# Optimization experiments

Measured on AMD Instinct MI355X. Metric: run time of the kernel, lower is better.

The kernel has to match this reference:

```python
import jax, jax.numpy as jnp
import numpy as np

B, L, D, H = 4, 2048, 1024, 16
DK = D // H  # 64


def setup_inputs() -> dict:
    key = jax.random.key(0)
    ks = jax.random.split(key, 8)
    s = 0.05
    return {
        "query": jax.random.normal(ks[0], (B, L, D), jnp.float32),
        "key": jax.random.normal(ks[1], (B, L, D), jnp.float32),
        "value": jax.random.normal(ks[2], (B, L, D), jnp.float32),
        "mask": jnp.ones((B, L, L), jnp.int32),
        "Wq": jax.random.normal(ks[3], (D, DK), jnp.float32) * s,
        "Wk": jax.random.normal(ks[4], (D, DK), jnp.float32) * s,
        "Wv": jax.random.normal(ks[5], (D, DK), jnp.float32) * s,
        "Wo": jax.random.normal(ks[6], (H * DK, D), jnp.float32) * s,
    }


def reference(query, key, value, mask, Wq, Wk, Wv, Wo):
    # Single-head projections (the torch module projects once, then reuses
    # the SAME q/k/v for every head, producing num_heads identical outputs).
    q = jnp.einsum("bld,dk->blk", query, Wq)   # [B, L, DK]
    k = jnp.einsum("bld,dk->blk", key, Wk)
    v = jnp.einsum("bld,dk->blk", value, Wv)
    scale = 1.0 / jnp.sqrt(jnp.asarray(DK, q.dtype))
    scores = jnp.einsum("bqk,bsk->bqs", q, k) * scale  # [B, L, L]
    scores = jnp.where(mask == 0, -jnp.inf, scores)
    p = jax.nn.softmax(scores, axis=-1)
    head = jnp.einsum("bqs,bsk->bqk", p, v)    # [B, L, DK]
    # Concatenation of H identical heads == tile along last dim.
    out = jnp.tile(head, (1, 1, H))             # [B, L, H*DK]
    return jnp.einsum("blh,hd->bld", out, Wo)
```

## Files before the change

### kernel.cpp

```cpp
#include <hip/hip_runtime.h>
#include <hip/hip_bf16.h>

#define Bb 4
#define Ll 2048
#define Dd 1024
#define DKk 64
#define BL (Bb*Ll)
#define G_SPLIT 8
#define KSPLIT 4

typedef __attribute__((ext_vector_type(4))) float f32x4;
typedef __attribute__((ext_vector_type(8))) short bf16x8;

__device__ __forceinline__ unsigned short f2bf(float x) {
  unsigned int u = __builtin_bit_cast(unsigned int, x);
  u += 0x7fffu + ((u >> 16) & 1u);
  return (unsigned short)(u >> 16);
}
__device__ __forceinline__ unsigned int pack2bf(float a, float b) {
  return (unsigned int)f2bf(a) | ((unsigned int)f2bf(b) << 16);
}

__global__ __launch_bounds__(256)
void prep_kernel(const float* __restrict__ Wq, const float* __restrict__ Wk,
                 const float* __restrict__ Wv, const float* __restrict__ Wo,
                 unsigned short* __restrict__ Wfq, unsigned short* __restrict__ Wfk,
                 unsigned short* __restrict__ Wfv, unsigned short* __restrict__ WoSumT) {
  int idx = blockIdx.x * 256 + threadIdx.x;
  if (idx < 3 * 65536) {
    int which = idx >> 16;
    int r = idx & 65535;
    int n = r & 63, k = r >> 6;
    const float* W = which == 0 ? Wq : (which == 1 ? Wk : Wv);
    unsigned short* Wf = which == 0 ? Wfq : (which == 1 ? Wfk : Wfv);
    const int t = n >> 4, lr = n & 15;
    const int kidx = k >> 5, g = (k >> 3) & 3, e = k & 7;
    Wf[(size_t)(((kidx * 4 + t) * 4 + g) * 128) + lr * 8 + e] = f2bf(W[(size_t)k * 64 + n]);
  } else {
    int r = idx - 3 * 65536;
    int d = r & 1023, k = r >> 10;
    float s = 0.f;
#pragma unroll
    for (int h = 0; h < 16; ++h) s += Wo[(size_t)(h * 64 + k) * 1024 + d];
    WoSumT[(size_t)d * 64 + k] = f2bf(s);
  }
}

__global__ __launch_bounds__(256)
void maskpack_kernel(const int* __restrict__ mask, unsigned long long* __restrict__ BM) {
  const int wid = (blockIdx.x * 256 + threadIdx.x) >> 6;
  const int lane = threadIdx.x & 63;
  const int nw = (gridDim.x * 256) >> 6;
  for (int task = wid; task < BL * 8; task += nw) {
    const int4 m = *(const int4*)(mask + (size_t)task * 256 + lane * 4);
    unsigned long long b0 = __ballot(m.x != 0);
    unsigned long long b1 = __ballot(m.y != 0);
    unsigned long long b2 = __ballot(m.z != 0);
    unsigned long long b3 = __ballot(m.w != 0);
    unsigned long long v = lane == 0 ? b0 : lane == 1 ? b1 : lane == 2 ? b2 : b3;
    if (lane < 4) BM[(size_t)task * 4 + lane] = v;
  }
}

__global__ __launch_bounds__(128)
void proj_kernel(const float* __restrict__ query, const float* __restrict__ key,
                 const float* __restrict__ value,
                 const unsigned short* __restrict__ Wfq, const unsigned short* __restrict__ Wfk,
                 const unsigned short* __restrict__ Wfv,
                 float* __restrict__ Pp) {
  const int which = blockIdx.y;
  const int ks = blockIdx.z;
  const float* X = which == 0 ? query : (which == 1 ? key : value);
  const unsigned short* Wf = which == 0 ? Wfq : (which == 1 ? Wfk : Wfv);
  const int R0 = blockIdx.x * 32;

  __shared__ __align__(16) unsigned short Xl[32 * 72];

  const int tid = threadIdx.x;
  const int lane = tid & 63;
  const int w = tid >> 6;
  const int g = lane >> 4, lr = lane & 15;

  f32x4 acc[4];
#pragma unroll
  for (int t = 0; t < 4; ++t) acc[t] = (f32x4){0.f, 0.f, 0.f, 0.f};

#pragma unroll
  for (int it = 0; it < 4; ++it) {
    const int K0 = ks * 256 + it * 64;
    if (it) __syncthreads();
#pragma unroll
    for (int i = 0; i < 4; ++i) {
      int c = tid + 128 * i;
      int row = c >> 4, cc = c & 15;
      f32x4 v = *(const f32x4*)(X + (size_t)(R0 + row) * 1024 + K0 + cc * 4);
      uint2 pv;
      pv.x = pack2bf(v[0], v[1]);
      pv.y = pack2bf(v[2], v[3]);
      *(uint2*)&Xl[row * 72 + cc * 4] = pv;
    }
    __syncthreads();
    const int kidx0 = K0 >> 5;
#pragma unroll
    for (int kh = 0; kh < 2; ++kh) {
      bf16x8 a = *(const bf16x8*)&Xl[(w * 16 + lr) * 72 + kh * 32 + g * 8];
#pragma unroll
      for (int t = 0; t < 4; ++t) {
        bf16x8 b = *(const bf16x8*)(Wf + (size_t)(((kidx0 + kh) * 4 + t) * 4 + g) * 128 + lr * 8);
        acc[t] = __builtin_amdgcn_mfma_f32_16x16x32_bf16(a, b, acc[t], 0, 0, 0);
      }
    }
  }

  float* pb = Pp + ((size_t)(which * KSPLIT + ks) * BL + R0 + w * 16) * 64;
#pragma unroll
  for (int t = 0; t < 4; ++t)
#pragma unroll
    for (int i = 0; i < 4; ++i)
      pb[(g * 4 + i) * 64 + t * 16 + lr] = acc[t][i];
}

__global__ __launch_bounds__(256)
void projcomb_kernel(const float* __restrict__ Pp,
                     unsigned short* __restrict__ Qp, unsigned short* __restrict__ Kf,
                     unsigned short* __restrict__ Vf) {
  const int which = blockIdx.y;
  int idx = blockIdx.x * 256 + threadIdx.x;
  int row = idx >> 4, c0 = (idx & 15) * 4;
  const float* base = Pp + ((size_t)which * KSPLIT * BL + row) * 64 + c0;
  f32x4 s = (f32x4){0.f, 0.f, 0.f, 0.f};
#pragma unroll
  for (int gg = 0; gg < KSPLIT; ++gg) {
    f32x4 a = *(const f32x4*)(base + (size_t)gg * BL * 64);
    s[0] += a[0]; s[1] += a[1]; s[2] += a[2]; s[3] += a[3];
  }
  const int b = row >> 11, sl = row & 2047;
  if (which == 0) {
    uint2 pv;
    pv.x = pack2bf(s[0], s[1]);
    pv.y = pack2bf(s[2], s[3]);
    *(uint2*)(Qp + (size_t)row * 64 + c0) = pv;
  } else if (which == 1) {
    const int c = (sl >> 4) & 3, lr = sl & 15, tile = b * 32 + (sl >> 6);
    const int gg = c0 >> 3, e0 = c0 & 7;
    uint2 pv;
    pv.x = pack2bf(s[0], s[1]);
    pv.y = pack2bf(s[2], s[3]);
    *(uint2*)(Kf + (size_t)tile * 4096 + (c * 8 + gg) * 128 + lr * 8 + e0) = pv;
  } else {
    const int h = (sl >> 5) & 1, g2 = (sl >> 3) & 3, e = sl & 7, tile = b * 32 + (sl >> 6);
#pragma unroll
    for (int j = 0; j < 4; ++j) {
      int dk = c0 + j, t = dk >> 4, lrv = dk & 15;
      Vf[(size_t)tile * 4096 + ((t * 2 + h) * 4 + g2) * 128 + lrv * 8 + e] = f2bf(s[j]);
    }
  }
}

__global__ __launch_bounds__(128, 4)
void attn_kernel(const unsigned short* __restrict__ Qp, const unsigned short* __restrict__ Kf,
                 const unsigned short* __restrict__ Vf, const unsigned long long* __restrict__ BM,
                 float* __restrict__ Opart, float* __restrict__ lpart) {
  const int q0 = blockIdx.x * 32;
  const int gy = blockIdx.y;
  const int b = q0 >> 11;
  const int tid = threadIdx.x, lane = tid & 63, w = tid >> 6;
  const int g = lane >> 4, lr = lane & 15;

  const unsigned short* qrow = Qp + (size_t)(q0 + w * 16 + lr) * 64;
  bf16x8 qf0 = *(const bf16x8*)(qrow + g * 8);
  bf16x8 qf1 = *(const bf16x8*)(qrow + 32 + g * 8);

  const unsigned long long* bm = BM + ((size_t)(q0 + w * 16 + lr) * 8 + gy) * 4;
  const unsigned long long W0 = bm[0], W1 = bm[1], W2 = bm[2], W3 = bm[3];

  f32x4 o[4];
#pragma unroll
  for (int t = 0; t < 4; ++t) o[t] = (f32x4){0.f, 0.f, 0.f, 0.f};
  float lsum = 0.f;

  const unsigned short* Kt = Kf + (size_t)(b * 32 + gy * 4) * 4096;
  const unsigned short* Vt = Vf + (size_t)(b * 32 + gy * 4) * 4096;

#pragma unroll
  for (int st = 0; st < 4; ++st) {
    const unsigned short* Kts = Kt + st * 4096;
    const unsigned short* Vts = Vt + st * 4096;

    bf16x8 kf0[4], kf1[4];
#pragma unroll
    for (int c = 0; c < 4; ++c) {
      kf0[c] = *(const bf16x8*)(Kts + (c * 8 + g) * 128 + lr * 8);
      kf1[c] = *(const bf16x8*)(Kts + (c * 8 + 4 + g) * 128 + lr * 8);
    }

    uint2 packs[4];
#pragma unroll
    for (int c = 0; c < 4; ++c) {
      f32x4 a4 = (f32x4){0.f, 0.f, 0.f, 0.f};
      a4 = __builtin_amdgcn_mfma_f32_16x16x32_bf16(kf0[c], qf0, a4, 0, 0, 0);
      a4 = __builtin_amdgcn_mfma_f32_16x16x32_bf16(kf1[c], qf1, a4, 0, 0, 0);
      const int j = st * 16 + 4 * c + g;
      float p0 = ((W0 >> j) & 1) ? __expf(a4[0] * 0.125f) : 0.f;
      float p1 = ((W1 >> j) & 1) ? __expf(a4[1] * 0.125f) : 0.f;
      float p2 = ((W2 >> j) & 1) ? __expf(a4[2] * 0.125f) : 0.f;
      float p3 = ((W3 >> j) & 1) ? __expf(a4[3] * 0.125f) : 0.f;
      lsum += (p0 + p1) + (p2 + p3);
      packs[c].x = pack2bf(p0, p1);
      packs[c].y = pack2bf(p2, p3);
    }

#pragma unroll
    for (int h = 0; h < 2; ++h) {
      const int srcLo = lr + ((g & 1) << 5);
      const int srcHi = srcLo + 16;
      uint2 pl0 = packs[2 * h], pl1 = packs[2 * h + 1];
      unsigned a0x = __shfl((int)pl0.x, srcLo), a0y = __shfl((int)pl0.y, srcLo);
      unsigned a1x = __shfl((int)pl1.x, srcLo), a1y = __shfl((int)pl1.y, srcLo);
      unsigned b0x = __shfl((int)pl0.x, srcHi), b0y = __shfl((int)pl0.y, srcHi);
      unsigned b1x = __shfl((int)pl1.x, srcHi), b1y = __shfl((int)pl1.y, srcHi);
      const bool hisel = ((g >> 1) & 1) != 0;
      uint4 bb;
      bb.x = hisel ? a1x : a0x;
      bb.y = hisel ? a1y : a0y;
      bb.z = hisel ? b1x : b0x;
      bb.w = hisel ? b1y : b0y;
      bf16x8 pb = __builtin_bit_cast(bf16x8, bb);
#pragma unroll
      for (int t = 0; t < 4; ++t) {
        bf16x8 av = *(const bf16x8*)(Vts + ((t * 2 + h) * 4 + g) * 128 + lr * 8);
        o[t] = __builtin_amdgcn_mfma_f32_16x16x32_bf16(av, pb, o[t], 0, 0, 0);
      }
    }
  }

  lsum += __shfl_xor(lsum, 16);
  lsum += __shfl_xor(lsum, 32);

  float* Ob = Opart + ((size_t)gy * BL + q0 + w * 16 + lr) * 64;
#pragma unroll
  for (int t = 0; t < 4; ++t)
    *(f32x4*)(Ob + t * 16 + g * 4) = o[t];
  if (lane < 16)
    lpart[(size_t)gy * BL + q0 + w * 16 + lane] = lsum;
}

__global__ __launch_bounds__(256)
void combine_kernel(const float* __restrict__ Opart, const float* __restrict__ lpart,
                    unsigned short* __restrict__ Hp) {
  int idx = blockIdx.x * 256 + threadIdx.x;
  int q = idx >> 4, c0 = (idx & 15) * 4;
  float l = 0.f;
#pragma unroll
  for (int gg = 0; gg < G_SPLIT; ++gg) l += lpart[(size_t)gg * BL + q];
  float inv = 1.f / l;
  f32x4 s = (f32x4){0.f, 0.f, 0.f, 0.f};
#pragma unroll
  for (int gg = 0; gg < G_SPLIT; ++gg) {
    f32x4 a = *(const f32x4*)(Opart + ((size_t)gg * BL + q) * 64 + c0);
    s[0] += a[0]; s[1] += a[1]; s[2] += a[2]; s[3] += a[3];
  }
  uint2 pv;
  pv.x = pack2bf(s[0] * inv, s[1] * inv);
  pv.y = pack2bf(s[2] * inv, s[3] * inv);
  *(uint2*)(Hp + (size_t)q * 64 + c0) = pv;
}

__global__ __launch_bounds__(256)
void oproj_kernel(const unsigned short* __restrict__ Hp,
                  const unsigned short* __restrict__ WoSumT, float* __restrict__ out) {
  const int R0 = blockIdx.x * 64;
  const int n0 = blockIdx.y * 256;
  __shared__ __align__(16) unsigned short Hl[64 * 72];
  __shared__ __align__(16) unsigned short Wl[256 * 72];
  const int tid = threadIdx.x, lane = tid & 63, w = tid >> 6;
  const int g = lane >> 4, lr = lane & 15;

#pragma unroll
  for (int i = 0; i < 2; ++i) {
    int c = tid + 256 * i;
    int row = c >> 3, cc = c & 7;
    *(uint4*)&Hl[row * 72 + cc * 8] = *(const uint4*)(Hp + (size_t)(R0 + row) * 64 + cc * 8);
  }
#pragma unroll
  for (int i = 0; i < 8; ++i) {
    int c = tid + 256 * i;
    int row = c >> 3, cc = c & 7;
    *(uint4*)&Wl[row * 72 + cc * 8] = *(const uint4*)(WoSumT + (size_t)(n0 + row) * 64 + cc * 8);
  }
  __syncthreads();

  f32x4 acc[16];
#pragma unroll
  for (int t = 0; t < 16; ++t) acc[t] = (f32x4){0.f, 0.f, 0.f, 0.f};
#pragma unroll
  for (int kh = 0; kh < 2; ++kh) {
    bf16x8 a = *(const bf16x8*)&Hl[(w * 16 + lr) * 72 + kh * 32 + g * 8];
#pragma unroll
    for (int t = 0; t < 16; ++t) {
      bf16x8 bb = *(const bf16x8*)&Wl[(t * 16 + lr) * 72 + kh * 32 + g * 8];
      acc[t] = __builtin_amdgcn_mfma_f32_16x16x32_bf16(a, bb, acc[t], 0, 0, 0);
    }
  }
  float* ob = out + (size_t)(R0 + w * 16 + g * 4) * 1024 + n0 + lr;
#pragma unroll
  for (int t = 0; t < 16; ++t)
#pragma unroll
    for (int i = 0; i < 4; ++i)
      ob[(size_t)i * 1024 + t * 16] = acc[t][i];
}

extern "C" void kernel_launch(void* const* d_in, const int* in_sizes, int n_in,
                              void* d_out, int out_size, void* d_ws, size_t ws_size,
                              hipStream_t stream) {
  const float* query = (const float*)d_in[0];
  const float* key   = (const float*)d_in[1];
  const float* value = (const float*)d_in[2];
  const int*   mask  = (const int*)d_in[3];
  const float* Wq    = (const float*)d_in[4];
  const float* Wk    = (const float*)d_in[5];
  const float* Wv    = (const float*)d_in[6];
  const float* Wo    = (const float*)d_in[7];
  float* out = (float*)d_out;

  unsigned short* Qp   = (unsigned short*)d_ws;
  unsigned short* Kf   = Qp + (size_t)BL * 64;
  unsigned short* Vf   = Kf + (size_t)BL * 64;
  unsigned short* Wfq  = Vf + (size_t)BL * 64;
  unsigned short* Wfk  = Wfq + 65536;
  unsigned short* Wfv  = Wfk + 65536;
  unsigned short* WoSumT = Wfv + 65536;
  float* lpart = (float*)(WoSumT + 65536);
  float* scratch = lpart + (size_t)G_SPLIT * BL;
  float* Pp = scratch;
  float* Opart = scratch;
  unsigned long long* BM = (unsigned long long*)(scratch + (size_t)G_SPLIT * BL * 64);
  unsigned short* Hp = Qp;

  hipLaunchKernelGGL(prep_kernel, dim3(1024), dim3(256), 0, stream,
                     Wq, Wk, Wv, Wo, Wfq, Wfk, Wfv, WoSumT);
  hipLaunchKernelGGL(proj_kernel, dim3(256, 3, KSPLIT), dim3(128), 0, stream,
                     query, key, value, Wfq, Wfk, Wfv, Pp);
  hipLaunchKernelGGL(projcomb_kernel, dim3(BL * 16 / 256, 3), dim3(256), 0, stream,
                     Pp, Qp, Kf, Vf);
  hipLaunchKernelGGL(maskpack_kernel, dim3(2048), dim3(256), 0, stream,
                     mask, BM);
  hipLaunchKernelGGL(attn_kernel, dim3(BL / 32, G_SPLIT), dim3(128), 0, stream,
                     Qp, Kf, Vf, BM, Opart, lpart);
  hipLaunchKernelGGL(combine_kernel, dim3(BL * 16 / 256), dim3(256), 0, stream,
                     Opart, lpart, Hp);
  hipLaunchKernelGGL(oproj_kernel, dim3(128, 4), dim3(256), 0, stream,
                     Hp, WoSumT, out);
}
```

Baseline: 82.74 us.

## Pre-convert projection inputs to MFMA-tiled bf16 and reduce K-split in LDS

Replaces the split-K projection kernel and its fp32 partial-sum combine pass. For each of Q, K and V, a new kernel first converts the input to bf16 in an MFMA fragment layout. A 512-thread GEMM kernel then splits K across eight waves and reduces the partials in shared memory before writing the bf16 Q/K/V layouts directly. This removes the fp32 partial buffer round trip through global memory. In exchange it adds an extra bf16 copy of each input, six launches instead of two, and a serialized loop that reuses one scratch buffer for all three inputs.

```diff
diff --git a/kernel.cpp b/kernel.cpp
--- a/kernel.cpp
+++ b/kernel.cpp
@@ -7,7 +7,6 @@
 #define DKk 64
 #define BL (Bb*Ll)
 #define G_SPLIT 8
-#define KSPLIT 4
 
 typedef __attribute__((ext_vector_type(4))) float f32x4;
 typedef __attribute__((ext_vector_type(8))) short bf16x8;
@@ -34,8 +33,8 @@
     const float* W = which == 0 ? Wq : (which == 1 ? Wk : Wv);
     unsigned short* Wf = which == 0 ? Wfq : (which == 1 ? Wfk : Wfv);
     const int t = n >> 4, lr = n & 15;
-    const int kidx = k >> 5, g = (k >> 3) & 3, e = k & 7;
-    Wf[(size_t)(((kidx * 4 + t) * 4 + g) * 128) + lr * 8 + e] = f2bf(W[(size_t)k * 64 + n]);
+    const int ks = k >> 5, g = (k >> 3) & 3, e = k & 7;
+    Wf[(size_t)(((ks * 4 + t) * 4 + g) * 128) + lr * 8 + e] = f2bf(W[(size_t)k * 64 + n]);
   } else {
     int r = idx - 3 * 65536;
     int d = r & 1023, k = r >> 10;
@@ -43,6 +42,83 @@
 #pragma unroll
     for (int h = 0; h < 16; ++h) s += Wo[(size_t)(h * 64 + k) * 1024 + d];
     WoSumT[(size_t)d * 64 + k] = f2bf(s);
+  }
+}
+
+__global__ __launch_bounds__(256)
+void xprep_kernel(const float* __restrict__ X, unsigned short* __restrict__ Xf) {
+  int gid = blockIdx.x * 256 + threadIdx.x;
+  int r = gid >> 7, kc = gid & 127;
+  const float* src = X + (size_t)r * 1024 + kc * 8;
+  f32x4 a = *(const f32x4*)src;
+  f32x4 b2 = *(const f32x4*)(src + 4);
+  uint4 p;
+  p.x = pack2bf(a[0], a[1]);
+  p.y = pack2bf(a[2], a[3]);
+  p.z = pack2bf(b2[0], b2[1]);
+  p.w = pack2bf(b2[2], b2[3]);
+  int rt = r >> 4, lr = r & 15, ks = kc >> 2, g = kc & 3;
+  *(uint4*)(Xf + (size_t)(rt * 32 + ks) * 512 + (g * 16 + lr) * 8) = p;
+}
+
+__global__ __launch_bounds__(512)
+void pgemm_kernel(const unsigned short* __restrict__ Xf, const unsigned short* __restrict__ Wf,
+                  const int which, unsigned short* __restrict__ Qp,
+                  unsigned short* __restrict__ Kf, unsigned short* __restrict__ Vf) {
+  __shared__ float Lc[8][4][64][4];
+  const int rt = blockIdx.x;
+  const int tid = threadIdx.x, w = tid >> 6, lane = tid & 63;
+  const int g = lane >> 4, lr = lane & 15;
+
+  f32x4 acc[4];
+#pragma unroll
+  for (int t = 0; t < 4; ++t) acc[t] = (f32x4){0.f, 0.f, 0.f, 0.f};
+
+  const unsigned short* xb = Xf + (size_t)(rt * 32 + w * 4) * 512 + lane * 8;
+#pragma unroll
+  for (int j = 0; j < 4; ++j) {
+    bf16x8 a = *(const bf16x8*)(xb + j * 512);
+    const int ks = w * 4 + j;
+#pragma unroll
+    for (int t = 0; t < 4; ++t) {
+      bf16x8 b = *(const bf16x8*)(Wf + (size_t)(ks * 16 + t * 4 + g) * 128 + lr * 8);
+      acc[t] = __builtin_amdgcn_mfma_f32_16x16x32_bf16(a, b, acc[t], 0, 0, 0);
+    }
+  }
+
+#pragma unroll
+  for (int t = 0; t < 4; ++t) *(f32x4*)&Lc[w][t][lane][0] = acc[t];
+  __syncthreads();
+  if (w < 4) {
+    f32x4 s = (f32x4){0.f, 0.f, 0.f, 0.f};
+#pragma unroll
+    for (int w2 = 0; w2 < 8; ++w2) {
+      f32x4 v = *(const f32x4*)&Lc[w2][w][lane][0];
+      s = s + v;
+    }
+    const int dk = w * 16 + lr;
+    if (which == 0) {
+#pragma unroll
+      for (int i = 0; i < 4; ++i)
+        Qp[(size_t)(rt * 16 + 4 * g + i) * 64 + dk] = f2bf(s[i]);
+    } else if (which == 1) {
+#pragma unroll
+      for (int i = 0; i < 4; ++i) {
+        const int sg = rt * 16 + 4 * g + i;
+        const int b = sg >> 11, sl = sg & 2047;
+        const int tile = b * 32 + (sl >> 6), c = (sl >> 4) & 3, lrk = sl & 15;
+        Kf[(size_t)tile * 4096 + (c * 8 + (dk >> 3)) * 128 + lrk * 8 + (dk & 7)] = f2bf(s[i]);
+      }
+    } else {
+#pragma unroll
+      for (int i = 0; i < 4; ++i) {
+        const int sg = rt * 16 + 4 * g + i;
+        const int b = sg >> 11, sl = sg & 2047;
+        const int tile = b * 32 + (sl >> 6);
+        const int h = (sl >> 5) & 1, g2 = (sl >> 3) & 3, e2 = sl & 7;
+        Vf[(size_t)tile * 4096 + ((w * 2 + h) * 4 + g2) * 128 + lr * 8 + e2] = f2bf(s[i]);
+      }
+    }
   }
 }
 
@@ -59,101 +135,6 @@
     unsigned long long b3 = __ballot(m.w != 0);
     unsigned long long v = lane == 0 ? b0 : lane == 1 ? b1 : lane == 2 ? b2 : b3;
     if (lane < 4) BM[(size_t)task * 4 + lane] = v;
-  }
-}
-
-__global__ __launch_bounds__(128)
-void proj_kernel(const float* __restrict__ query, const float* __restrict__ key,
-                 const float* __restrict__ value,
-                 const unsigned short* __restrict__ Wfq, const unsigned short* __restrict__ Wfk,
-                 const unsigned short* __restrict__ Wfv,
-                 float* __restrict__ Pp) {
-  const int which = blockIdx.y;
-  const int ks = blockIdx.z;
-  const float* X = which == 0 ? query : (which == 1 ? key : value);
-  const unsigned short* Wf = which == 0 ? Wfq : (which == 1 ? Wfk : Wfv);
-  const int R0 = blockIdx.x * 32;
-
-  __shared__ __align__(16) unsigned short Xl[32 * 72];
-
-  const int tid = threadIdx.x;
-  const int lane = tid & 63;
-  const int w = tid >> 6;
-  const int g = lane >> 4, lr = lane & 15;
-
-  f32x4 acc[4];
-#pragma unroll
-  for (int t = 0; t < 4; ++t) acc[t] = (f32x4){0.f, 0.f, 0.f, 0.f};
-
-#pragma unroll
-  for (int it = 0; it < 4; ++it) {
-    const int K0 = ks * 256 + it * 64;
-    if (it) __syncthreads();
-#pragma unroll
-    for (int i = 0; i < 4; ++i) {
-      int c = tid + 128 * i;
-      int row = c >> 4, cc = c & 15;
-      f32x4 v = *(const f32x4*)(X + (size_t)(R0 + row) * 1024 + K0 + cc * 4);
-      uint2 pv;
-      pv.x = pack2bf(v[0], v[1]);
-      pv.y = pack2bf(v[2], v[3]);
-      *(uint2*)&Xl[row * 72 + cc * 4] = pv;
-    }
-    __syncthreads();
-    const int kidx0 = K0 >> 5;
-#pragma unroll
-    for (int kh = 0; kh < 2; ++kh) {
-      bf16x8 a = *(const bf16x8*)&Xl[(w * 16 + lr) * 72 + kh * 32 + g * 8];
-#pragma unroll
-      for (int t = 0; t < 4; ++t) {
-        bf16x8 b = *(const bf16x8*)(Wf + (size_t)(((kidx0 + kh) * 4 + t) * 4 + g) * 128 + lr * 8);
-        acc[t] = __builtin_amdgcn_mfma_f32_16x16x32_bf16(a, b, acc[t], 0, 0, 0);
-      }
-    }
-  }
-
-  float* pb = Pp + ((size_t)(which * KSPLIT + ks) * BL + R0 + w * 16) * 64;
-#pragma unroll
-  for (int t = 0; t < 4; ++t)
-#pragma unroll
-    for (int i = 0; i < 4; ++i)
-      pb[(g * 4 + i) * 64 + t * 16 + lr] = acc[t][i];
-}
-
-__global__ __launch_bounds__(256)
-void projcomb_kernel(const float* __restrict__ Pp,
-                     unsigned short* __restrict__ Qp, unsigned short* __restrict__ Kf,
-                     unsigned short* __restrict__ Vf) {
-  const int which = blockIdx.y;
-  int idx = blockIdx.x * 256 + threadIdx.x;
-  int row = idx >> 4, c0 = (idx & 15) * 4;
-  const float* base = Pp + ((size_t)which * KSPLIT * BL + row) * 64 + c0;
-  f32x4 s = (f32x4){0.f, 0.f, 0.f, 0.f};
-#pragma unroll
-  for (int gg = 0; gg < KSPLIT; ++gg) {
-    f32x4 a = *(const f32x4*)(base + (size_t)gg * BL * 64);
-    s[0] += a[0]; s[1] += a[1]; s[2] += a[2]; s[3] += a[3];
-  }
-  const int b = row >> 11, sl = row & 2047;
-  if (which == 0) {
-    uint2 pv;
-    pv.x = pack2bf(s[0], s[1]);
-    pv.y = pack2bf(s[2], s[3]);
-    *(uint2*)(Qp + (size_t)row * 64 + c0) = pv;
-  } else if (which == 1) {
-    const int c = (sl >> 4) & 3, lr = sl & 15, tile = b * 32 + (sl >> 6);
-    const int gg = c0 >> 3, e0 = c0 & 7;
-    uint2 pv;
-    pv.x = pack2bf(s[0], s[1]);
-    pv.y = pack2bf(s[2], s[3]);
-    *(uint2*)(Kf + (size_t)tile * 4096 + (c * 8 + gg) * 128 + lr * 8 + e0) = pv;
-  } else {
-    const int h = (sl >> 5) & 1, g2 = (sl >> 3) & 3, e = sl & 7, tile = b * 32 + (sl >> 6);
-#pragma unroll
-    for (int j = 0; j < 4; ++j) {
-      int dk = c0 + j, t = dk >> 4, lrv = dk & 15;
-      Vf[(size_t)tile * 4096 + ((t * 2 + h) * 4 + g2) * 128 + lrv * 8 + e] = f2bf(s[j]);
-    }
   }
 }
 
@@ -332,17 +313,21 @@
   unsigned short* WoSumT = Wfv + 65536;
   float* lpart = (float*)(WoSumT + 65536);
   float* scratch = lpart + (size_t)G_SPLIT * BL;
-  float* Pp = scratch;
   float* Opart = scratch;
   unsigned long long* BM = (unsigned long long*)(scratch + (size_t)G_SPLIT * BL * 64);
+  unsigned short* Xf = (unsigned short*)scratch;
   unsigned short* Hp = Qp;
 
   hipLaunchKernelGGL(prep_kernel, dim3(1024), dim3(256), 0, stream,
                      Wq, Wk, Wv, Wo, Wfq, Wfk, Wfv, WoSumT);
-  hipLaunchKernelGGL(proj_kernel, dim3(256, 3, KSPLIT), dim3(128), 0, stream,
-                     query, key, value, Wfq, Wfk, Wfv, Pp);
-  hipLaunchKernelGGL(projcomb_kernel, dim3(BL * 16 / 256, 3), dim3(256), 0, stream,
-                     Pp, Qp, Kf, Vf);
+  const float* Xs[3] = {query, key, value};
+  const unsigned short* Wfs[3] = {Wfq, Wfk, Wfv};
+  for (int which = 0; which < 3; ++which) {
+    hipLaunchKernelGGL(xprep_kernel, dim3(4096), dim3(256), 0, stream,
+                       Xs[which], Xf);
+    hipLaunchKernelGGL(pgemm_kernel, dim3(512), dim3(512), 0, stream,
+                       Xf, Wfs[which], which, Qp, Kf, Vf);
+  }
   hipLaunchKernelGGL(maskpack_kernel, dim3(2048), dim3(256), 0, stream,
                      mask, BM);
   hipLaunchKernelGGL(attn_kernel, dim3(BL / 32, G_SPLIT), dim3(128), 0, stream,
```

Result: slower. 110.9 us (+34.1%).

## Restructure projection kernel: 16-row tiles, 512-wide K chunks, one output tile per wave

Applied to the files above, without the earlier changes.

The projection GEMM now stages a 16x512 input slab into shared memory once per block with a single barrier, and each of four waves computes one 16-column output tile over the whole K chunk, using two accumulators to hide MFMA latency. K is split two ways instead of four, so the partial-sum buffer and the combine pass read half as much. The aim is fewer barriers, less partial-sum traffic and more blocks in flight. The cost is that weight fragments are no longer shared across tiles within a wave, and each block uses more shared memory.

```diff
diff --git a/kernel.cpp b/kernel.cpp
--- a/kernel.cpp
+++ b/kernel.cpp
@@ -7,7 +7,7 @@
 #define DKk 64
 #define BL (Bb*Ll)
 #define G_SPLIT 8
-#define KSPLIT 4
+#define KSPLIT 2
 
 typedef __attribute__((ext_vector_type(4))) float f32x4;
 typedef __attribute__((ext_vector_type(8))) short bf16x8;
@@ -34,8 +34,8 @@
     const float* W = which == 0 ? Wq : (which == 1 ? Wk : Wv);
     unsigned short* Wf = which == 0 ? Wfq : (which == 1 ? Wfk : Wfv);
     const int t = n >> 4, lr = n & 15;
-    const int kidx = k >> 5, g = (k >> 3) & 3, e = k & 7;
-    Wf[(size_t)(((kidx * 4 + t) * 4 + g) * 128) + lr * 8 + e] = f2bf(W[(size_t)k * 64 + n]);
+    const int ks = k >> 5, g = (k >> 3) & 3, e = k & 7;
+    Wf[(size_t)(((ks * 4 + t) * 4 + g) * 128) + lr * 8 + e] = f2bf(W[(size_t)k * 64 + n]);
   } else {
     int r = idx - 3 * 65536;
     int d = r & 1023, k = r >> 10;
@@ -43,6 +43,94 @@
 #pragma unroll
     for (int h = 0; h < 16; ++h) s += Wo[(size_t)(h * 64 + k) * 1024 + d];
     WoSumT[(size_t)d * 64 + k] = f2bf(s);
+  }
+}
+
+__global__ __launch_bounds__(256)
+void proj_kernel(const float* __restrict__ query, const float* __restrict__ key,
+                 const float* __restrict__ value,
+                 const unsigned short* __restrict__ Wfq, const unsigned short* __restrict__ Wfk,
+                 const unsigned short* __restrict__ Wfv,
+                 float* __restrict__ Pp) {
+  const int which = blockIdx.y;
+  const int ks2 = blockIdx.z;
+  const float* X = which == 0 ? query : (which == 1 ? key : value);
+  const unsigned short* Wf = which == 0 ? Wfq : (which == 1 ? Wfk : Wfv);
+  const int R0 = blockIdx.x * 16;
+  const int K0 = ks2 * 512;
+
+  __shared__ __align__(16) unsigned short Xl[16 * 520];
+
+  const int tid = threadIdx.x, w = tid >> 6, lane = tid & 63;
+  const int g = lane >> 4, lr = lane & 15;
+
+#pragma unroll
+  for (int i = 0; i < 8; ++i) {
+    int c = tid + 256 * i;
+    int row = c >> 7, c4 = c & 127;
+    f32x4 v = *(const f32x4*)(X + (size_t)(R0 + row) * 1024 + K0 + c4 * 4);
+    uint2 p;
+    p.x = pack2bf(v[0], v[1]);
+    p.y = pack2bf(v[2], v[3]);
+    *(uint2*)&Xl[row * 520 + c4 * 4] = p;
+  }
+  __syncthreads();
+
+  f32x4 acc0 = (f32x4){0.f, 0.f, 0.f, 0.f};
+  f32x4 acc1 = (f32x4){0.f, 0.f, 0.f, 0.f};
+  const unsigned short* xrow = &Xl[lr * 520 + g * 8];
+  const unsigned short* wfb = Wf + (size_t)((ks2 * 16 * 4 + w) * 4 + g) * 128 + lr * 8;
+#pragma unroll
+  for (int ks = 0; ks < 16; ks += 2) {
+    bf16x8 a0 = *(const bf16x8*)(xrow + ks * 32);
+    bf16x8 b0 = *(const bf16x8*)(wfb + (size_t)ks * 2048);
+    acc0 = __builtin_amdgcn_mfma_f32_16x16x32_bf16(a0, b0, acc0, 0, 0, 0);
+    bf16x8 a1 = *(const bf16x8*)(xrow + (ks + 1) * 32);
+    bf16x8 b1 = *(const bf16x8*)(wfb + (size_t)(ks + 1) * 2048);
+    acc1 = __builtin_amdgcn_mfma_f32_16x16x32_bf16(a1, b1, acc1, 0, 0, 0);
+  }
+  f32x4 acc = acc0 + acc1;
+
+  float* pb = Pp + ((size_t)(which * KSPLIT + ks2) * BL + R0) * 64;
+#pragma unroll
+  for (int i = 0; i < 4; ++i)
+    pb[(4 * g + i) * 64 + w * 16 + lr] = acc[i];
+}
+
+__global__ __launch_bounds__(256)
+void projcomb_kernel(const float* __restrict__ Pp,
+                     unsigned short* __restrict__ Qp, unsigned short* __restrict__ Kf,
+                     unsigned short* __restrict__ Vf) {
+  const int which = blockIdx.y;
+  int idx = blockIdx.x * 256 + threadIdx.x;
+  int row = idx >> 4, c0 = (idx & 15) * 4;
+  const float* base = Pp + ((size_t)which * KSPLIT * BL + row) * 64 + c0;
+  f32x4 s = (f32x4){0.f, 0.f, 0.f, 0.f};
+#pragma unroll
+  for (int gg = 0; gg < KSPLIT; ++gg) {
+    f32x4 a = *(const f32x4*)(base + (size_t)gg * BL * 64);
+    s[0] += a[0]; s[1] += a[1]; s[2] += a[2]; s[3] += a[3];
+  }
+  const int b = row >> 11, sl = row & 2047;
+  if (which == 0) {
+    uint2 pv;
+    pv.x = pack2bf(s[0], s[1]);
+    pv.y = pack2bf(s[2], s[3]);
+    *(uint2*)(Qp + (size_t)row * 64 + c0) = pv;
+  } else if (which == 1) {
+    const int c = (sl >> 4) & 3, lrk = sl & 15, tile = b * 32 + (sl >> 6);
+    const int gg = c0 >> 3, e0 = c0 & 7;
+    uint2 pv;
+    pv.x = pack2bf(s[0], s[1]);
+    pv.y = pack2bf(s[2], s[3]);
+    *(uint2*)(Kf + (size_t)tile * 4096 + (c * 8 + gg) * 128 + lrk * 8 + e0) = pv;
+  } else {
+    const int h = (sl >> 5) & 1, g2 = (sl >> 3) & 3, e = sl & 7, tile = b * 32 + (sl >> 6);
+#pragma unroll
+    for (int j = 0; j < 4; ++j) {
+      int dk = c0 + j, t = dk >> 4, lrv = dk & 15;
+      Vf[(size_t)tile * 4096 + ((t * 2 + h) * 4 + g2) * 128 + lrv * 8 + e] = f2bf(s[j]);
+    }
   }
 }
 
@@ -59,101 +147,6 @@
     unsigned long long b3 = __ballot(m.w != 0);
     unsigned long long v = lane == 0 ? b0 : lane == 1 ? b1 : lane == 2 ? b2 : b3;
     if (lane < 4) BM[(size_t)task * 4 + lane] = v;
-  }
-}
-
-__global__ __launch_bounds__(128)
-void proj_kernel(const float* __restrict__ query, const float* __restrict__ key,
-                 const float* __restrict__ value,
-                 const unsigned short* __restrict__ Wfq, const unsigned short* __restrict__ Wfk,
-                 const unsigned short* __restrict__ Wfv,
-                 float* __restrict__ Pp) {
-  const int which = blockIdx.y;
-  const int ks = blockIdx.z;
-  const float* X = which == 0 ? query : (which == 1 ? key : value);
-  const unsigned short* Wf = which == 0 ? Wfq : (which == 1 ? Wfk : Wfv);
-  const int R0 = blockIdx.x * 32;
-
-  __shared__ __align__(16) unsigned short Xl[32 * 72];
-
-  const int tid = threadIdx.x;
-  const int lane = tid & 63;
-  const int w = tid >> 6;
-  const int g = lane >> 4, lr = lane & 15;
-
-  f32x4 acc[4];
-#pragma unroll
-  for (int t = 0; t < 4; ++t) acc[t] = (f32x4){0.f, 0.f, 0.f, 0.f};
-
-#pragma unroll
-  for (int it = 0; it < 4; ++it) {
-    const int K0 = ks * 256 + it * 64;
-    if (it) __syncthreads();
-#pragma unroll
-    for (int i = 0; i < 4; ++i) {
-      int c = tid + 128 * i;
-      int row = c >> 4, cc = c & 15;
-      f32x4 v = *(const f32x4*)(X + (size_t)(R0 + row) * 1024 + K0 + cc * 4);
-      uint2 pv;
-      pv.x = pack2bf(v[0], v[1]);
-      pv.y = pack2bf(v[2], v[3]);
-      *(uint2*)&Xl[row * 72 + cc * 4] = pv;
-    }
-    __syncthreads();
-    const int kidx0 = K0 >> 5;
-#pragma unroll
-    for (int kh = 0; kh < 2; ++kh) {
-      bf16x8 a = *(const bf16x8*)&Xl[(w * 16 + lr) * 72 + kh * 32 + g * 8];
-#pragma unroll
-      for (int t = 0; t < 4; ++t) {
-        bf16x8 b = *(const bf16x8*)(Wf + (size_t)(((kidx0 + kh) * 4 + t) * 4 + g) * 128 + lr * 8);
-        acc[t] = __builtin_amdgcn_mfma_f32_16x16x32_bf16(a, b, acc[t], 0, 0, 0);
-      }
-    }
-  }
-
-  float* pb = Pp + ((size_t)(which * KSPLIT + ks) * BL + R0 + w * 16) * 64;
-#pragma unroll
-  for (int t = 0; t < 4; ++t)
-#pragma unroll
-    for (int i = 0; i < 4; ++i)
-      pb[(g * 4 + i) * 64 + t * 16 + lr] = acc[t][i];
-}
-
-__global__ __launch_bounds__(256)
-void projcomb_kernel(const float* __restrict__ Pp,
-                     unsigned short* __restrict__ Qp, unsigned short* __restrict__ Kf,
-                     unsigned short* __restrict__ Vf) {
-  const int which = blockIdx.y;
-  int idx = blockIdx.x * 256 + threadIdx.x;
-  int row = idx >> 4, c0 = (idx & 15) * 4;
-  const float* base = Pp + ((size_t)which * KSPLIT * BL + row) * 64 + c0;
-  f32x4 s = (f32x4){0.f, 0.f, 0.f, 0.f};
-#pragma unroll
-  for (int gg = 0; gg < KSPLIT; ++gg) {
-    f32x4 a = *(const f32x4*)(base + (size_t)gg * BL * 64);
-    s[0] += a[0]; s[1] += a[1]; s[2] += a[2]; s[3] += a[3];
-  }
-  const int b = row >> 11, sl = row & 2047;
-  if (which == 0) {
-    uint2 pv;
-    pv.x = pack2bf(s[0], s[1]);
-    pv.y = pack2bf(s[2], s[3]);
-    *(uint2*)(Qp + (size_t)row * 64 + c0) = pv;
-  } else if (which == 1) {
-    const int c = (sl >> 4) & 3, lr = sl & 15, tile = b * 32 + (sl >> 6);
-    const int gg = c0 >> 3, e0 = c0 & 7;
-    uint2 pv;
-    pv.x = pack2bf(s[0], s[1]);
-    pv.y = pack2bf(s[2], s[3]);
-    *(uint2*)(Kf + (size_t)tile * 4096 + (c * 8 + gg) * 128 + lr * 8 + e0) = pv;
-  } else {
-    const int h = (sl >> 5) & 1, g2 = (sl >> 3) & 3, e = sl & 7, tile = b * 32 + (sl >> 6);
-#pragma unroll
-    for (int j = 0; j < 4; ++j) {
-      int dk = c0 + j, t = dk >> 4, lrv = dk & 15;
-      Vf[(size_t)tile * 4096 + ((t * 2 + h) * 4 + g2) * 128 + lrv * 8 + e] = f2bf(s[j]);
-    }
   }
 }
 
@@ -339,7 +332,7 @@
 
   hipLaunchKernelGGL(prep_kernel, dim3(1024), dim3(256), 0, stream,
                      Wq, Wk, Wv, Wo, Wfq, Wfk, Wfv, WoSumT);
-  hipLaunchKernelGGL(proj_kernel, dim3(256, 3, KSPLIT), dim3(128), 0, stream,
+  hipLaunchKernelGGL(proj_kernel, dim3(512, 3, KSPLIT), dim3(256), 0, stream,
                      query, key, value, Wfq, Wfk, Wfv, Pp);
   hipLaunchKernelGGL(projcomb_kernel, dim3(BL * 16 / 256, 3), dim3(256), 0, stream,
                      Pp, Qp, Kf, Vf);
```

Measured after the change: 85.42 us. 3.2% more time.
